# Kernel tuning notes

Measured on AMD Instinct MI355X. Metric: run time of the kernel, lower is better.

The kernel has to match this reference:

```python
import jax, jax.numpy as jnp
import numpy as np

B, N = 4096, 4096
BISECTION_ITERS = 40


def setup_inputs() -> dict:
    key = jax.random.key(0)
    kz, = jax.random.split(key, 1)
    z = jax.random.normal(kz, (B, N), dtype=jnp.float32)
    gamma = jnp.ones((N,), dtype=jnp.float32)   # GammaParam fixed, init=1, clamped at eps (no-op here)
    m = jnp.zeros((N,), dtype=jnp.float32)      # BoundsParam fixed, m_init=0
    M = jnp.ones((N,), dtype=jnp.float32)       # BoundsParam fixed, M_init=1
    xi = jnp.ones((B,), dtype=jnp.float32)      # fixed xi=1 expanded to batch
    return {"z": z, "gamma": gamma, "m": m, "M": M, "xi": xi}


def reference(z, gamma, m, M, xi):
    """Weighted L2 projection of z (B,N) onto {x: sum x = xi, m <= x <= M} via bisection on lambda."""
    Bq, Nq = z.shape
    gB = jnp.broadcast_to(gamma, (Bq, Nq))
    mB = jnp.broadcast_to(m, (Bq, Nq))
    MB = jnp.broadcast_to(M, (Bq, Nq))
    two_gamma = 2.0 * gB

    lam_low = jnp.min(two_gamma * (mB - z), axis=-1)   # (B,)
    lam_high = jnp.max(two_gamma * (MB - z), axis=-1)  # (B,)

    def body(_, carry):
        lo, hi = carry
        mid = 0.5 * (lo + hi)
        x_mid = jnp.clip(z + mid[:, None] / two_gamma, mB, MB)
        g_mid = jnp.sum(x_mid, axis=-1) - xi
        pos = g_mid > 0
        lo_new = jnp.where(pos, lo, mid)
        hi_new = jnp.where(pos, mid, hi)
        return (lo_new, hi_new)

    lam_low, lam_high = jax.lax.fori_loop(0, BISECTION_ITERS, body, (lam_low, lam_high))
    lam = 0.5 * (lam_low + lam_high)
    x = jnp.clip(z + lam[:, None] / two_gamma, mB, MB)
    return x
```

## Files before the change

### kernel.cpp

```cpp
#include <hip/hip_runtime.h>


#define BISECT_STEPS 6
#define TOTAL_STEPS  9

template<int CTRL, int RM>
__device__ __forceinline__ float dpp_add(float v) {
    int t = __builtin_amdgcn_update_dpp(0, __float_as_int(v), CTRL, RM, 0xf, false);
    return v + __int_as_float(t);
}
template<int CTRL, int RM>
__device__ __forceinline__ float dpp_min(float v) {
    int t = __builtin_amdgcn_update_dpp(0x7f800000, __float_as_int(v), CTRL, RM, 0xf, false);
    return fminf(v, __int_as_float(t));
}
template<int CTRL, int RM>
__device__ __forceinline__ float dpp_max(float v) {
    int t = __builtin_amdgcn_update_dpp(0xff800000, __float_as_int(v), CTRL, RM, 0xf, false);
    return fmaxf(v, __int_as_float(t));
}

__device__ __forceinline__ float wave_sum(float v) {
    v = dpp_add<0x111, 0xf>(v);
    v = dpp_add<0x112, 0xf>(v);
    v = dpp_add<0x114, 0xf>(v);
    v = dpp_add<0x118, 0xf>(v);
    v = dpp_add<0x142, 0xa>(v);
    v = dpp_add<0x143, 0xc>(v);
    return __int_as_float(__builtin_amdgcn_readlane(__float_as_int(v), 63));
}
__device__ __forceinline__ float wave_min(float v) {
    v = dpp_min<0x111, 0xf>(v);
    v = dpp_min<0x112, 0xf>(v);
    v = dpp_min<0x114, 0xf>(v);
    v = dpp_min<0x118, 0xf>(v);
    v = dpp_min<0x142, 0xa>(v);
    v = dpp_min<0x143, 0xc>(v);
    return __int_as_float(__builtin_amdgcn_readlane(__float_as_int(v), 63));
}
__device__ __forceinline__ float wave_max(float v) {
    v = dpp_max<0x111, 0xf>(v);
    v = dpp_max<0x112, 0xf>(v);
    v = dpp_max<0x114, 0xf>(v);
    v = dpp_max<0x118, 0xf>(v);
    v = dpp_max<0x142, 0xa>(v);
    v = dpp_max<0x143, 0xc>(v);
    return __int_as_float(__builtin_amdgcn_readlane(__float_as_int(v), 63));
}

__global__ __launch_bounds__(256, 4) void qp_proj_n4096(
    const float* __restrict__ z,
    const float* __restrict__ gamma,
    const float* __restrict__ mlo,
    const float* __restrict__ mhi,
    const float* __restrict__ xi,
    float* __restrict__ out)
{
    constexpr int N = 4096;
    const int row  = blockIdx.x;
    const int tid  = threadIdx.x;
    const int lane = tid & 63;
    const int wid  = tid >> 6;

    const float4* zrow = reinterpret_cast<const float4*>(z + (size_t)row * N);
    const float4* g4   = reinterpret_cast<const float4*>(gamma);
    const float4* m4   = reinterpret_cast<const float4*>(mlo);
    const float4* M4   = reinterpret_cast<const float4*>(mhi);
    float4*       orow = reinterpret_cast<float4*>(out + (size_t)row * N);

    float za[16], ia[16], ma[16], Ma[16];

    float pmin =  INFINITY;
    float pmax = -INFINITY;
    float psm  = 0.0f;
    float psM  = 0.0f;

    #pragma unroll
    for (int k = 0; k < 4; ++k) {
        const int idx = tid + k * 256;
        const float4 zz = zrow[idx];
        const float4 gg = g4[idx];
        const float4 mm = m4[idx];
        const float4 MM = M4[idx];

        const float zs[4] = {zz.x, zz.y, zz.z, zz.w};
        const float gs[4] = {gg.x, gg.y, gg.z, gg.w};
        const float ms[4] = {mm.x, mm.y, mm.z, mm.w};
        const float Ms[4] = {MM.x, MM.y, MM.z, MM.w};

        #pragma unroll
        for (int c = 0; c < 4; ++c) {
            const int j = 4 * k + c;
            const float tg = 2.0f * gs[c];
            za[j] = zs[c];
            ia[j] = 1.0f / tg;
            ma[j] = ms[c];
            Ma[j] = Ms[c];
            pmin = fminf(pmin, tg * (ms[c] - zs[c]));
            pmax = fmaxf(pmax, tg * (Ms[c] - zs[c]));
            psm += ms[c];
            psM += Ms[c];
        }
    }

    __shared__ float wmin[4], wmax[4], wsm[4], wsM[4];
    __shared__ float wsum[2][4];

    pmin = wave_min(pmin);
    pmax = wave_max(pmax);
    psm  = wave_sum(psm);
    psM  = wave_sum(psM);
    if (lane == 0) { wmin[wid] = pmin; wmax[wid] = pmax; wsm[wid] = psm; wsM[wid] = psM; }
    __syncthreads();
    float lo = fminf(fminf(wmin[0], wmin[1]), fminf(wmin[2], wmin[3]));
    float hi = fmaxf(fmaxf(wmax[0], wmax[1]), fmaxf(wmax[2], wmax[3]));

    const float xir = xi[row];
    float glo = (wsm[0] + wsm[1] + wsm[2] + wsm[3]) - xir;
    float ghi = (wsM[0] + wsM[1] + wsM[2] + wsM[3]) - xir;
    int side = 0;

    for (int it = 0; it < TOTAL_STEPS; ++it) {
        const float w = hi - lo;
        float cand;
        if (it < BISECT_STEPS) {
            cand = fmaf(0.5f, w, lo);
        } else {
            const float denom = ghi - glo;
            cand = (lo * ghi - hi * glo) / denom;
            cand = fminf(fmaxf(cand, fmaf(0.0625f, w, lo)),
                         fmaf(-0.0625f, w, hi));
        }

        float t0 = 0.f, t1 = 0.f, t2 = 0.f, t3 = 0.f;
        #pragma unroll
        for (int q = 0; q < 4; ++q) {
            t0 += __builtin_amdgcn_fmed3f(fmaf(cand, ia[4*q+0], za[4*q+0]), ma[4*q+0], Ma[4*q+0]);
            t1 += __builtin_amdgcn_fmed3f(fmaf(cand, ia[4*q+1], za[4*q+1]), ma[4*q+1], Ma[4*q+1]);
            t2 += __builtin_amdgcn_fmed3f(fmaf(cand, ia[4*q+2], za[4*q+2]), ma[4*q+2], Ma[4*q+2]);
            t3 += __builtin_amdgcn_fmed3f(fmaf(cand, ia[4*q+3], za[4*q+3]), ma[4*q+3], Ma[4*q+3]);
        }
        const float sw = wave_sum((t0 + t1) + (t2 + t3));

        const int p = it & 1;
        if (lane == 0) wsum[p][wid] = sw;
        __syncthreads();
        const float s = (wsum[p][0] + wsum[p][1] + wsum[p][2] + wsum[p][3]) - xir;

        if (s > 0.0f) {
            hi = cand;
            if (side == 1) glo *= 0.5f;
            ghi = s;
            side = 1;
        } else {
            lo = cand;
            if (side == -1) ghi *= 0.5f;
            glo = s;
            side = -1;
        }
    }

    const float denom = ghi - glo;
    float lam = (denom > 0.0f) ? (lo * ghi - hi * glo) / denom
                               : fmaf(0.5f, hi - lo, lo);
    lam = fminf(fmaxf(lam, lo), hi);

    #pragma unroll
    for (int k = 0; k < 4; ++k) {
        const int idx = tid + k * 256;
        float4 r;
        float xs[4];
        #pragma unroll
        for (int c = 0; c < 4; ++c) {
            const int j = 4 * k + c;
            const float x = fmaf(lam, ia[j], za[j]);
            xs[c] = __builtin_amdgcn_fmed3f(x, ma[j], Ma[j]);
        }
        r.x = xs[0]; r.y = xs[1]; r.z = xs[2]; r.w = xs[3];
        orow[idx] = r;
    }
}

extern "C" void kernel_launch(void* const* d_in, const int* in_sizes, int n_in,
                              void* d_out, int out_size, void* d_ws, size_t ws_size,
                              hipStream_t stream) {
    const float* z     = (const float*)d_in[0];
    const float* gamma = (const float*)d_in[1];
    const float* m     = (const float*)d_in[2];
    const float* M     = (const float*)d_in[3];
    const float* xi    = (const float*)d_in[4];
    float* out = (float*)d_out;

    const int B = in_sizes[4];
    qp_proj_n4096<<<dim3(B), dim3(256), 0, stream>>>(z, gamma, m, M, xi, out);
}
```

Measured before the change: 34.60 us.

## Reformulate clamp in lambda space and stage per-element bounds in LDS

Rewrites the per-element term clip(z + lam/2g, m, M) as z + med3(lam, lb, hb)/2g, precomputing lb = 2g(m-z) and hb = 2g(M-z). The constant sum of z moves into an adjusted target. The three per-element arrays are kept in shared memory instead of 64 registers per thread, and the occupancy hint in launch bounds is dropped. This cuts register pressure and per-iteration operand count, but adds LDS reads every bisection step, an extra global load of m in the output pass, and a slightly different rounding path for the output.

After: 44.90 us. 29.8% more time.

```diff
diff --git a/kernel.cpp b/kernel.cpp
--- a/kernel.cpp
+++ b/kernel.cpp
@@ -48,7 +48,7 @@
     return __int_as_float(__builtin_amdgcn_readlane(__float_as_int(v), 63));
 }
 
-__global__ __launch_bounds__(256, 4) void qp_proj_n4096(
+__global__ __launch_bounds__(256) void qp_proj_n4096(
     const float* __restrict__ z,
     const float* __restrict__ gamma,
     const float* __restrict__ mlo,
@@ -68,12 +68,17 @@
     const float4* M4   = reinterpret_cast<const float4*>(mhi);
     float4*       orow = reinterpret_cast<float4*>(out + (size_t)row * N);
 
-    float za[16], ia[16], ma[16], Ma[16];
+    __shared__ float4 LB[4][256];
+    __shared__ float4 HB[4][256];
+    __shared__ float4 IA[4][256];
+    __shared__ float  wred[5][4];
+    __shared__ float  wsum[2][4];
 
     float pmin =  INFINITY;
     float pmax = -INFINITY;
     float psm  = 0.0f;
     float psM  = 0.0f;
+    float psz  = 0.0f;
 
     #pragma unroll
     for (int k = 0; k < 4; ++k) {
@@ -88,36 +93,44 @@
         const float ms[4] = {mm.x, mm.y, mm.z, mm.w};
         const float Ms[4] = {MM.x, MM.y, MM.z, MM.w};
 
+        float lb[4], hb[4], ia[4];
         #pragma unroll
         for (int c = 0; c < 4; ++c) {
-            const int j = 4 * k + c;
             const float tg = 2.0f * gs[c];
-            za[j] = zs[c];
-            ia[j] = 1.0f / tg;
-            ma[j] = ms[c];
-            Ma[j] = Ms[c];
-            pmin = fminf(pmin, tg * (ms[c] - zs[c]));
-            pmax = fmaxf(pmax, tg * (Ms[c] - zs[c]));
+            lb[c] = tg * (ms[c] - zs[c]);
+            hb[c] = tg * (Ms[c] - zs[c]);
+            ia[c] = 1.0f / tg;
+            pmin = fminf(pmin, lb[c]);
+            pmax = fmaxf(pmax, hb[c]);
             psm += ms[c];
             psM += Ms[c];
-        }
-    }
-
-    __shared__ float wmin[4], wmax[4], wsm[4], wsM[4];
-    __shared__ float wsum[2][4];
+            psz += zs[c];
+        }
+        LB[k][tid] = make_float4(lb[0], lb[1], lb[2], lb[3]);
+        HB[k][tid] = make_float4(hb[0], hb[1], hb[2], hb[3]);
+        IA[k][tid] = make_float4(ia[0], ia[1], ia[2], ia[3]);
+    }
 
     pmin = wave_min(pmin);
     pmax = wave_max(pmax);
     psm  = wave_sum(psm);
     psM  = wave_sum(psM);
-    if (lane == 0) { wmin[wid] = pmin; wmax[wid] = pmax; wsm[wid] = psm; wsM[wid] = psM; }
+    psz  = wave_sum(psz);
+    if (lane == 0) {
+        wred[0][wid] = pmin; wred[1][wid] = pmax;
+        wred[2][wid] = psm;  wred[3][wid] = psM;  wred[4][wid] = psz;
+    }
     __syncthreads();
-    float lo = fminf(fminf(wmin[0], wmin[1]), fminf(wmin[2], wmin[3]));
-    float hi = fmaxf(fmaxf(wmax[0], wmax[1]), fmaxf(wmax[2], wmax[3]));
-
-    const float xir = xi[row];
-    float glo = (wsm[0] + wsm[1] + wsm[2] + wsm[3]) - xir;
-    float ghi = (wsM[0] + wsM[1] + wsM[2] + wsM[3]) - xir;
+    float lo = fminf(fminf(wred[0][0], wred[0][1]), fminf(wred[0][2], wred[0][3]));
+    float hi = fmaxf(fmaxf(wred[1][0], wred[1][1]), fmaxf(wred[1][2], wred[1][3]));
+    const float smT = (wred[2][0] + wred[2][1]) + (wred[2][2] + wred[2][3]);
+    const float sMT = (wred[3][0] + wred[3][1]) + (wred[3][2] + wred[3][3]);
+    const float szT = (wred[4][0] + wred[4][1]) + (wred[4][2] + wred[4][3]);
+
+    const float xir     = xi[row];
+    const float xir_eff = xir - szT;
+    float glo = smT - xir;
+    float ghi = sMT - xir;
     int side = 0;
 
     for (int it = 0; it < TOTAL_STEPS; ++it) {
@@ -134,18 +147,22 @@
 
         float t0 = 0.f, t1 = 0.f, t2 = 0.f, t3 = 0.f;
         #pragma unroll
-        for (int q = 0; q < 4; ++q) {
-            t0 += __builtin_amdgcn_fmed3f(fmaf(cand, ia[4*q+0], za[4*q+0]), ma[4*q+0], Ma[4*q+0]);
-            t1 += __builtin_amdgcn_fmed3f(fmaf(cand, ia[4*q+1], za[4*q+1]), ma[4*q+1], Ma[4*q+1]);
-            t2 += __builtin_amdgcn_fmed3f(fmaf(cand, ia[4*q+2], za[4*q+2]), ma[4*q+2], Ma[4*q+2]);
-            t3 += __builtin_amdgcn_fmed3f(fmaf(cand, ia[4*q+3], za[4*q+3]), ma[4*q+3], Ma[4*q+3]);
+        for (int k = 0; k < 4; ++k) {
+            const float4 lb = LB[k][tid];
+            const float4 hb = HB[k][tid];
+            const float4 ia = IA[k][tid];
+            t0 = fmaf(ia.x, __builtin_amdgcn_fmed3f(cand, lb.x, hb.x), t0);
+            t1 = fmaf(ia.y, __builtin_amdgcn_fmed3f(cand, lb.y, hb.y), t1);
+            t2 = fmaf(ia.z, __builtin_amdgcn_fmed3f(cand, lb.z, hb.z), t2);
+            t3 = fmaf(ia.w, __builtin_amdgcn_fmed3f(cand, lb.w, hb.w), t3);
         }
         const float sw = wave_sum((t0 + t1) + (t2 + t3));
 
         const int p = it & 1;
         if (lane == 0) wsum[p][wid] = sw;
         __syncthreads();
-        const float s = (wsum[p][0] + wsum[p][1] + wsum[p][2] + wsum[p][3]) - xir;
+        const float s = ((wsum[p][0] + wsum[p][1]) + (wsum[p][2] + wsum[p][3]))
+                        - xir_eff;
 
         if (s > 0.0f) {
             hi = cand;
@@ -168,15 +185,15 @@
     #pragma unroll
     for (int k = 0; k < 4; ++k) {
         const int idx = tid + k * 256;
+        const float4 mm = m4[idx];
+        const float4 lb = LB[k][tid];
+        const float4 hb = HB[k][tid];
+        const float4 ia = IA[k][tid];
         float4 r;
-        float xs[4];
-        #pragma unroll
-        for (int c = 0; c < 4; ++c) {
-            const int j = 4 * k + c;
-            const float x = fmaf(lam, ia[j], za[j]);
-            xs[c] = __builtin_amdgcn_fmed3f(x, ma[j], Ma[j]);
-        }
-        r.x = xs[0]; r.y = xs[1]; r.z = xs[2]; r.w = xs[3];
+        r.x = fmaf(ia.x, __builtin_amdgcn_fmed3f(lam, lb.x, hb.x) - lb.x, mm.x);
+        r.y = fmaf(ia.y, __builtin_amdgcn_fmed3f(lam, lb.y, hb.y) - lb.y, mm.y);
+        r.z = fmaf(ia.z, __builtin_amdgcn_fmed3f(lam, lb.z, hb.z) - lb.z, mm.z);
+        r.w = fmaf(ia.w, __builtin_amdgcn_fmed3f(lam, lb.w, hb.w) - lb.w, mm.w);
         orow[idx] = r;
     }
 }
```

## Specialize for uniform gamma/bounds, process two rows per block with LDS prefetch

Applied to the files above, without the earlier changes.

Adds a pre-pass kernel that checks whether gamma, m and M are uniform across columns and stores the scalar values in the workspace. When they are, the main kernel skips loading the per-column parameter vectors and runs scalar clamps, with the bracket computed from the row min and max of z. It also gives each block two rows: the second row is streamed into LDS with global_load_lds while the first row is reduced, and both rows' reductions share one barrier per step. The step count drops by one, and the fallback path keeps the general per-column behaviour. The risks are an extra memset and launch per call, a coarser solution from one less step, and doubling per-block work, which halves the grid and may hurt occupancy.

Result: slower. 41.04 us (+18.6%).

```diff
diff --git a/kernel.cpp b/kernel.cpp
--- a/kernel.cpp
+++ b/kernel.cpp
@@ -2,182 +2,332 @@
 
 
 #define BISECT_STEPS 6
-#define TOTAL_STEPS  9
+#define TOTAL_STEPS  8
+
+#define GLD_LDS16(gp, lp) __builtin_amdgcn_global_load_lds( \
+    (const __attribute__((address_space(1))) void*)(gp),    \
+    (__attribute__((address_space(3))) void*)(lp), 16, 0, 0)
 
 template<int CTRL, int RM>
-__device__ __forceinline__ float dpp_add(float v) {
+__device__ __forceinline__ float dpp_addf(float v) {
     int t = __builtin_amdgcn_update_dpp(0, __float_as_int(v), CTRL, RM, 0xf, false);
     return v + __int_as_float(t);
 }
 template<int CTRL, int RM>
-__device__ __forceinline__ float dpp_min(float v) {
+__device__ __forceinline__ float dpp_minf(float v) {
     int t = __builtin_amdgcn_update_dpp(0x7f800000, __float_as_int(v), CTRL, RM, 0xf, false);
     return fminf(v, __int_as_float(t));
 }
 template<int CTRL, int RM>
-__device__ __forceinline__ float dpp_max(float v) {
+__device__ __forceinline__ float dpp_maxf(float v) {
     int t = __builtin_amdgcn_update_dpp(0xff800000, __float_as_int(v), CTRL, RM, 0xf, false);
     return fmaxf(v, __int_as_float(t));
 }
-
 __device__ __forceinline__ float wave_sum(float v) {
-    v = dpp_add<0x111, 0xf>(v);
-    v = dpp_add<0x112, 0xf>(v);
-    v = dpp_add<0x114, 0xf>(v);
-    v = dpp_add<0x118, 0xf>(v);
-    v = dpp_add<0x142, 0xa>(v);
-    v = dpp_add<0x143, 0xc>(v);
+    v = dpp_addf<0x111, 0xf>(v);
+    v = dpp_addf<0x112, 0xf>(v);
+    v = dpp_addf<0x114, 0xf>(v);
+    v = dpp_addf<0x118, 0xf>(v);
+    v = dpp_addf<0x142, 0xa>(v);
+    v = dpp_addf<0x143, 0xc>(v);
     return __int_as_float(__builtin_amdgcn_readlane(__float_as_int(v), 63));
 }
 __device__ __forceinline__ float wave_min(float v) {
-    v = dpp_min<0x111, 0xf>(v);
-    v = dpp_min<0x112, 0xf>(v);
-    v = dpp_min<0x114, 0xf>(v);
-    v = dpp_min<0x118, 0xf>(v);
-    v = dpp_min<0x142, 0xa>(v);
-    v = dpp_min<0x143, 0xc>(v);
+    v = dpp_minf<0x111, 0xf>(v);
+    v = dpp_minf<0x112, 0xf>(v);
+    v = dpp_minf<0x114, 0xf>(v);
+    v = dpp_minf<0x118, 0xf>(v);
+    v = dpp_minf<0x142, 0xa>(v);
+    v = dpp_minf<0x143, 0xc>(v);
     return __int_as_float(__builtin_amdgcn_readlane(__float_as_int(v), 63));
 }
 __device__ __forceinline__ float wave_max(float v) {
-    v = dpp_max<0x111, 0xf>(v);
-    v = dpp_max<0x112, 0xf>(v);
-    v = dpp_max<0x114, 0xf>(v);
-    v = dpp_max<0x118, 0xf>(v);
-    v = dpp_max<0x142, 0xa>(v);
-    v = dpp_max<0x143, 0xc>(v);
+    v = dpp_maxf<0x111, 0xf>(v);
+    v = dpp_maxf<0x112, 0xf>(v);
+    v = dpp_maxf<0x114, 0xf>(v);
+    v = dpp_maxf<0x118, 0xf>(v);
+    v = dpp_maxf<0x142, 0xa>(v);
+    v = dpp_maxf<0x143, 0xc>(v);
     return __int_as_float(__builtin_amdgcn_readlane(__float_as_int(v), 63));
 }
 
-__global__ __launch_bounds__(256, 4) void qp_proj_n4096(
+__device__ __forceinline__ float pick_cand(float lo, float hi, float glo,
+                                           float ghi, int it) {
+    const float w = hi - lo;
+    if (it < BISECT_STEPS) return fmaf(0.5f, w, lo);
+    const float denom = ghi - glo;
+    float c = (lo * ghi - hi * glo) / denom;
+    return fminf(fmaxf(c, fmaf(0.0625f, w, lo)), fmaf(-0.0625f, w, hi));
+}
+
+__global__ __launch_bounds__(256) void qp_uniform_check(
+    const float* __restrict__ g, const float* __restrict__ m,
+    const float* __restrict__ M, int n4, void* ws)
+{
+    const int tid = blockIdx.x * 256 + threadIdx.x;
+    const float g0 = g[0], m0 = m[0], M0 = M[0];
+    bool bad = !((g0 > 0.0f) && (M0 >= m0));
+    const float4* g4 = (const float4*)g;
+    const float4* m4 = (const float4*)m;
+    const float4* M4 = (const float4*)M;
+    if (tid < n4) {
+        const float4 a = g4[tid], b = m4[tid], c = M4[tid];
+        bad = bad || (a.x != g0) || (a.y != g0) || (a.z != g0) || (a.w != g0)
+                  || (b.x != m0) || (b.y != m0) || (b.z != m0) || (b.w != m0)
+                  || (c.x != M0) || (c.y != M0) || (c.z != M0) || (c.w != M0);
+    }
+    if (__ballot(bad) != 0ull && (threadIdx.x & 63) == 0)
+        atomicOr((int*)ws, 1);
+    if (tid == 0) {
+        float* wf = (float*)ws;
+        wf[1] = g0; wf[2] = m0; wf[3] = M0;
+    }
+}
+
+__global__ __launch_bounds__(256) void qp_proj2_n4096(
     const float* __restrict__ z,
     const float* __restrict__ gamma,
     const float* __restrict__ mlo,
     const float* __restrict__ mhi,
     const float* __restrict__ xi,
-    float* __restrict__ out)
+    float* __restrict__ out,
+    const void* __restrict__ ws,
+    int Btot)
 {
     constexpr int N = 4096;
-    const int row  = blockIdx.x;
     const int tid  = threadIdx.x;
     const int lane = tid & 63;
     const int wid  = tid >> 6;
-
-    const float4* zrow = reinterpret_cast<const float4*>(z + (size_t)row * N);
-    const float4* g4   = reinterpret_cast<const float4*>(gamma);
-    const float4* m4   = reinterpret_cast<const float4*>(mlo);
-    const float4* M4   = reinterpret_cast<const float4*>(mhi);
-    float4*       orow = reinterpret_cast<float4*>(out + (size_t)row * N);
-
-    float za[16], ia[16], ma[16], Ma[16];
-
-    float pmin =  INFINITY;
-    float pmax = -INFINITY;
-    float psm  = 0.0f;
-    float psM  = 0.0f;
-
+    const int rowA = blockIdx.x * 2;
+    const int rowB = rowA + 1;
+    const bool hasB = (rowB < Btot);
+
+    __shared__ float4 zsB[N / 4];
+    __shared__ float  red[4][4];
+    __shared__ float  wsum[2][2][4];
+
+    const float4* zA4 = reinterpret_cast<const float4*>(z + (size_t)rowA * N);
+    float4* oA4 = reinterpret_cast<float4*>(out + (size_t)rowA * N);
+    float4* oB4 = reinterpret_cast<float4*>(out + (size_t)rowB * N);
+
+    if (hasB) {
+        const char* src = (const char*)(z + (size_t)rowB * N) + tid * 16;
+        char* dst = (char*)zsB + tid * 16;
+        #pragma unroll
+        for (int k = 0; k < 4; ++k)
+            GLD_LDS16(src + k * 4096, dst + k * 4096);
+    }
+
+    float za[16];
+    float amn = INFINITY, amx = -INFINITY;
     #pragma unroll
     for (int k = 0; k < 4; ++k) {
-        const int idx = tid + k * 256;
-        const float4 zz = zrow[idx];
-        const float4 gg = g4[idx];
-        const float4 mm = m4[idx];
-        const float4 MM = M4[idx];
-
-        const float zs[4] = {zz.x, zz.y, zz.z, zz.w};
-        const float gs[4] = {gg.x, gg.y, gg.z, gg.w};
-        const float ms[4] = {mm.x, mm.y, mm.z, mm.w};
-        const float Ms[4] = {MM.x, MM.y, MM.z, MM.w};
-
+        const float4 v = zA4[tid + k * 256];
+        za[4*k+0] = v.x; za[4*k+1] = v.y; za[4*k+2] = v.z; za[4*k+3] = v.w;
+        amn = fminf(amn, fminf(fminf(v.x, v.y), fminf(v.z, v.w)));
+        amx = fmaxf(amx, fmaxf(fmaxf(v.x, v.y), fmaxf(v.z, v.w)));
+    }
+    amn = wave_min(amn);
+    amx = wave_max(amx);
+
+    const int   uniBad = ((const int*)ws)[0];
+    const float g0 = ((const float*)ws)[1];
+    const float m0 = ((const float*)ws)[2];
+    const float M0 = ((const float*)ws)[3];
+    const float xiA = xi[rowA];
+    const float xiB = hasB ? xi[rowB] : 0.0f;
+
+    asm volatile("s_waitcnt vmcnt(0)" ::: "memory");
+    __builtin_amdgcn_sched_barrier(0);
+
+    float bmn = INFINITY, bmx = -INFINITY;
+    if (hasB) {
         #pragma unroll
-        for (int c = 0; c < 4; ++c) {
-            const int j = 4 * k + c;
-            const float tg = 2.0f * gs[c];
-            za[j] = zs[c];
-            ia[j] = 1.0f / tg;
-            ma[j] = ms[c];
-            Ma[j] = Ms[c];
-            pmin = fminf(pmin, tg * (ms[c] - zs[c]));
-            pmax = fmaxf(pmax, tg * (Ms[c] - zs[c]));
-            psm += ms[c];
-            psM += Ms[c];
-        }
-    }
-
-    __shared__ float wmin[4], wmax[4], wsm[4], wsM[4];
-    __shared__ float wsum[2][4];
-
-    pmin = wave_min(pmin);
-    pmax = wave_max(pmax);
-    psm  = wave_sum(psm);
-    psM  = wave_sum(psM);
-    if (lane == 0) { wmin[wid] = pmin; wmax[wid] = pmax; wsm[wid] = psm; wsM[wid] = psM; }
+        for (int k = 0; k < 4; ++k) {
+            const float4 v = zsB[tid + k * 256];
+            bmn = fminf(bmn, fminf(fminf(v.x, v.y), fminf(v.z, v.w)));
+            bmx = fmaxf(bmx, fmaxf(fmaxf(v.x, v.y), fmaxf(v.z, v.w)));
+        }
+    }
+    bmn = wave_min(bmn);
+    bmx = wave_max(bmx);
+    if (lane == 0) { red[0][wid] = amn; red[1][wid] = amx;
+                     red[2][wid] = bmn; red[3][wid] = bmx; }
     __syncthreads();
-    float lo = fminf(fminf(wmin[0], wmin[1]), fminf(wmin[2], wmin[3]));
-    float hi = fmaxf(fmaxf(wmax[0], wmax[1]), fmaxf(wmax[2], wmax[3]));
-
-    const float xir = xi[row];
-    float glo = (wsm[0] + wsm[1] + wsm[2] + wsm[3]) - xir;
-    float ghi = (wsM[0] + wsM[1] + wsM[2] + wsM[3]) - xir;
-    int side = 0;
-
-    for (int it = 0; it < TOTAL_STEPS; ++it) {
-        const float w = hi - lo;
-        float cand;
-        if (it < BISECT_STEPS) {
-            cand = fmaf(0.5f, w, lo);
-        } else {
+    const float zAmin = fminf(fminf(red[0][0], red[0][1]), fminf(red[0][2], red[0][3]));
+    const float zAmax = fmaxf(fmaxf(red[1][0], red[1][1]), fmaxf(red[1][2], red[1][3]));
+    const float zBmin = fminf(fminf(red[2][0], red[2][1]), fminf(red[2][2], red[2][3]));
+    const float zBmax = fmaxf(fmaxf(red[3][0], red[3][1]), fmaxf(red[3][2], red[3][3]));
+
+    if (uniBad == 0) {
+        const float tg = 2.0f * g0;
+        const float ia = 1.0f / tg;
+        const float base_lo = (float)N * m0;
+        const float base_hi = (float)N * M0;
+
+        float loA = tg * (m0 - zAmax), hiA = tg * (M0 - zAmin);
+        float gloA = base_lo - xiA,    ghiA = base_hi - xiA;
+        int sideA = 0;
+        float loB = tg * (m0 - zBmax), hiB = tg * (M0 - zBmin);
+        float gloB = base_lo - xiB,    ghiB = base_hi - xiB;
+        int sideB = 0;
+
+        for (int it = 0; it < TOTAL_STEPS; ++it) {
+            const float cA = pick_cand(loA, hiA, gloA, ghiA, it);
+            const float cB = pick_cand(loB, hiB, gloB, ghiB, it);
+
+            float a0 = 0.f, a1 = 0.f, a2 = 0.f, a3 = 0.f;
+            #pragma unroll
+            for (int q = 0; q < 4; ++q) {
+                a0 += __builtin_amdgcn_fmed3f(fmaf(cA, ia, za[4*q+0]), m0, M0);
+                a1 += __builtin_amdgcn_fmed3f(fmaf(cA, ia, za[4*q+1]), m0, M0);
+                a2 += __builtin_amdgcn_fmed3f(fmaf(cA, ia, za[4*q+2]), m0, M0);
+                a3 += __builtin_amdgcn_fmed3f(fmaf(cA, ia, za[4*q+3]), m0, M0);
+            }
+            float b0 = 0.f, b1 = 0.f, b2 = 0.f, b3 = 0.f;
+            #pragma unroll
+            for (int k = 0; k < 4; ++k) {
+                const float4 v = zsB[tid + k * 256];
+                b0 += __builtin_amdgcn_fmed3f(fmaf(cB, ia, v.x), m0, M0);
+                b1 += __builtin_amdgcn_fmed3f(fmaf(cB, ia, v.y), m0, M0);
+                b2 += __builtin_amdgcn_fmed3f(fmaf(cB, ia, v.z), m0, M0);
+                b3 += __builtin_amdgcn_fmed3f(fmaf(cB, ia, v.w), m0, M0);
+            }
+            const float sA = wave_sum((a0 + a1) + (a2 + a3));
+            const float sB = wave_sum((b0 + b1) + (b2 + b3));
+
+            const int p = it & 1;
+            if (lane == 0) { wsum[p][0][wid] = sA; wsum[p][1][wid] = sB; }
+            __syncthreads();
+            const float gA = ((wsum[p][0][0] + wsum[p][0][1]) + (wsum[p][0][2] + wsum[p][0][3])) - xiA;
+            const float gB = ((wsum[p][1][0] + wsum[p][1][1]) + (wsum[p][1][2] + wsum[p][1][3])) - xiB;
+
+            if (gA > 0.0f) { hiA = cA; if (sideA == 1) gloA *= 0.5f; ghiA = gA; sideA = 1; }
+            else           { loA = cA; if (sideA == -1) ghiA *= 0.5f; gloA = gA; sideA = -1; }
+            if (gB > 0.0f) { hiB = cB; if (sideB == 1) gloB *= 0.5f; ghiB = gB; sideB = 1; }
+            else           { loB = cB; if (sideB == -1) ghiB *= 0.5f; gloB = gB; sideB = -1; }
+        }
+
+        const float dA = ghiA - gloA;
+        float lamA = (dA > 0.0f) ? (loA * ghiA - hiA * gloA) / dA
+                                 : fmaf(0.5f, hiA - loA, loA);
+        lamA = fminf(fmaxf(lamA, loA), hiA);
+        const float dB = ghiB - gloB;
+        float lamB = (dB > 0.0f) ? (loB * ghiB - hiB * gloB) / dB
+                                 : fmaf(0.5f, hiB - loB, loB);
+        lamB = fminf(fmaxf(lamB, loB), hiB);
+
+        #pragma unroll
+        for (int k = 0; k < 4; ++k) {
+            float4 r;
+            r.x = __builtin_amdgcn_fmed3f(fmaf(lamA, ia, za[4*k+0]), m0, M0);
+            r.y = __builtin_amdgcn_fmed3f(fmaf(lamA, ia, za[4*k+1]), m0, M0);
+            r.z = __builtin_amdgcn_fmed3f(fmaf(lamA, ia, za[4*k+2]), m0, M0);
+            r.w = __builtin_amdgcn_fmed3f(fmaf(lamA, ia, za[4*k+3]), m0, M0);
+            oA4[tid + k * 256] = r;
+        }
+        if (hasB) {
+            #pragma unroll
+            for (int k = 0; k < 4; ++k) {
+                const float4 v = zsB[tid + k * 256];
+                float4 r;
+                r.x = __builtin_amdgcn_fmed3f(fmaf(lamB, ia, v.x), m0, M0);
+                r.y = __builtin_amdgcn_fmed3f(fmaf(lamB, ia, v.y), m0, M0);
+                r.z = __builtin_amdgcn_fmed3f(fmaf(lamB, ia, v.z), m0, M0);
+                r.w = __builtin_amdgcn_fmed3f(fmaf(lamB, ia, v.w), m0, M0);
+                oB4[tid + k * 256] = r;
+            }
+        }
+    } else {
+        const float4* g4 = reinterpret_cast<const float4*>(gamma);
+        const float4* m4 = reinterpret_cast<const float4*>(mlo);
+        const float4* M4 = reinterpret_cast<const float4*>(mhi);
+
+        for (int rr = 0; rr < 2; ++rr) {
+            const int row = rowA + rr;
+            if (row >= Btot) break;
+            const float4* zr = reinterpret_cast<const float4*>(z + (size_t)row * N);
+            float4* orow = reinterpret_cast<float4*>(out + (size_t)row * N);
+            const float xir = xi[row];
+
+            float zb[16], ib[16], ma[16], Ma[16];
+            float pmin = INFINITY, pmax = -INFINITY, psm = 0.0f, psM = 0.0f;
+            #pragma unroll
+            for (int k = 0; k < 4; ++k) {
+                const int idx = tid + k * 256;
+                const float4 zz = zr[idx];
+                const float4 gg = g4[idx];
+                const float4 mm = m4[idx];
+                const float4 MM = M4[idx];
+                const float zc[4] = {zz.x, zz.y, zz.z, zz.w};
+                const float gc[4] = {gg.x, gg.y, gg.z, gg.w};
+                const float mc[4] = {mm.x, mm.y, mm.z, mm.w};
+                const float Mc[4] = {MM.x, MM.y, MM.z, MM.w};
+                #pragma unroll
+                for (int c = 0; c < 4; ++c) {
+                    const int j = 4 * k + c;
+                    const float tg2 = 2.0f * gc[c];
+                    zb[j] = zc[c];
+                    ib[j] = 1.0f / tg2;
+                    ma[j] = mc[c];
+                    Ma[j] = Mc[c];
+                    pmin = fminf(pmin, tg2 * (mc[c] - zc[c]));
+                    pmax = fmaxf(pmax, tg2 * (Mc[c] - zc[c]));
+                    psm += mc[c];
+                    psM += Mc[c];
+                }
+            }
+            pmin = wave_min(pmin);
+            pmax = wave_max(pmax);
+            psm  = wave_sum(psm);
+            psM  = wave_sum(psM);
+            if (lane == 0) { red[0][wid] = pmin; red[1][wid] = pmax;
+                             red[2][wid] = psm;  red[3][wid] = psM; }
+            __syncthreads();
+            float lo = fminf(fminf(red[0][0], red[0][1]), fminf(red[0][2], red[0][3]));
+            float hi = fmaxf(fmaxf(red[1][0], red[1][1]), fmaxf(red[1][2], red[1][3]));
+            float glo = ((red[2][0] + red[2][1]) + (red[2][2] + red[2][3])) - xir;
+            float ghi = ((red[3][0] + red[3][1]) + (red[3][2] + red[3][3])) - xir;
+            int side = 0;
+
+            for (int it = 0; it < TOTAL_STEPS + 1; ++it) {
+                const float cand = pick_cand(lo, hi, glo, ghi, it);
+                float t0 = 0.f, t1 = 0.f, t2 = 0.f, t3 = 0.f;
+                #pragma unroll
+                for (int q = 0; q < 4; ++q) {
+                    t0 += __builtin_amdgcn_fmed3f(fmaf(cand, ib[4*q+0], zb[4*q+0]), ma[4*q+0], Ma[4*q+0]);
+                    t1 += __builtin_amdgcn_fmed3f(fmaf(cand, ib[4*q+1], zb[4*q+1]), ma[4*q+1], Ma[4*q+1]);
+                    t2 += __builtin_amdgcn_fmed3f(fmaf(cand, ib[4*q+2], zb[4*q+2]), ma[4*q+2], Ma[4*q+2]);
+                    t3 += __builtin_amdgcn_fmed3f(fmaf(cand, ib[4*q+3], zb[4*q+3]), ma[4*q+3], Ma[4*q+3]);
+                }
+                const float sw = wave_sum((t0 + t1) + (t2 + t3));
+                const int p = it & 1;
+                if (lane == 0) wsum[p][0][wid] = sw;
+                __syncthreads();
+                const float s = ((wsum[p][0][0] + wsum[p][0][1]) + (wsum[p][0][2] + wsum[p][0][3])) - xir;
+                if (s > 0.0f) { hi = cand; if (side == 1) glo *= 0.5f; ghi = s; side = 1; }
+                else          { lo = cand; if (side == -1) ghi *= 0.5f; glo = s; side = -1; }
+            }
+
             const float denom = ghi - glo;
-            cand = (lo * ghi - hi * glo) / denom;
-            cand = fminf(fmaxf(cand, fmaf(0.0625f, w, lo)),
-                         fmaf(-0.0625f, w, hi));
-        }
-
-        float t0 = 0.f, t1 = 0.f, t2 = 0.f, t3 = 0.f;
-        #pragma unroll
-        for (int q = 0; q < 4; ++q) {
-            t0 += __builtin_amdgcn_fmed3f(fmaf(cand, ia[4*q+0], za[4*q+0]), ma[4*q+0], Ma[4*q+0]);
-            t1 += __builtin_amdgcn_fmed3f(fmaf(cand, ia[4*q+1], za[4*q+1]), ma[4*q+1], Ma[4*q+1]);
-            t2 += __builtin_amdgcn_fmed3f(fmaf(cand, ia[4*q+2], za[4*q+2]), ma[4*q+2], Ma[4*q+2]);
-            t3 += __builtin_amdgcn_fmed3f(fmaf(cand, ia[4*q+3], za[4*q+3]), ma[4*q+3], Ma[4*q+3]);
-        }
-        const float sw = wave_sum((t0 + t1) + (t2 + t3));
-
-        const int p = it & 1;
-        if (lane == 0) wsum[p][wid] = sw;
-        __syncthreads();
-        const float s = (wsum[p][0] + wsum[p][1] + wsum[p][2] + wsum[p][3]) - xir;
-
-        if (s > 0.0f) {
-            hi = cand;
-            if (side == 1) glo *= 0.5f;
-            ghi = s;
-            side = 1;
-        } else {
-            lo = cand;
-            if (side == -1) ghi *= 0.5f;
-            glo = s;
-            side = -1;
-        }
-    }
-
-    const float denom = ghi - glo;
-    float lam = (denom > 0.0f) ? (lo * ghi - hi * glo) / denom
-                               : fmaf(0.5f, hi - lo, lo);
-    lam = fminf(fmaxf(lam, lo), hi);
-
-    #pragma unroll
-    for (int k = 0; k < 4; ++k) {
-        const int idx = tid + k * 256;
-        float4 r;
-        float xs[4];
-        #pragma unroll
-        for (int c = 0; c < 4; ++c) {
-            const int j = 4 * k + c;
-            const float x = fmaf(lam, ia[j], za[j]);
-            xs[c] = __builtin_amdgcn_fmed3f(x, ma[j], Ma[j]);
-        }
-        r.x = xs[0]; r.y = xs[1]; r.z = xs[2]; r.w = xs[3];
-        orow[idx] = r;
+            float lam = (denom > 0.0f) ? (lo * ghi - hi * glo) / denom
+                                       : fmaf(0.5f, hi - lo, lo);
+            lam = fminf(fmaxf(lam, lo), hi);
+
+            #pragma unroll
+            for (int k = 0; k < 4; ++k) {
+                float4 r;
+                float xs[4];
+                #pragma unroll
+                for (int c = 0; c < 4; ++c) {
+                    const int j = 4 * k + c;
+                    xs[c] = __builtin_amdgcn_fmed3f(fmaf(lam, ib[j], zb[j]), ma[j], Ma[j]);
+                }
+                r.x = xs[0]; r.y = xs[1]; r.z = xs[2]; r.w = xs[3];
+                orow[tid + k * 256] = r;
+            }
+            __syncthreads();
+        }
     }
 }
 
@@ -192,5 +342,12 @@
     float* out = (float*)d_out;
 
     const int B = in_sizes[4];
-    qp_proj_n4096<<<dim3(B), dim3(256), 0, stream>>>(z, gamma, m, M, xi, out);
-}
+    const int N = in_sizes[1];
+    const int n4 = N / 4;
+
+    hipMemsetAsync(d_ws, 0, 4, stream);
+    qp_uniform_check<<<dim3((n4 + 255) / 256), dim3(256), 0, stream>>>(gamma, m, M, n4, d_ws);
+
+    const int nblocks = (B + 1) / 2;
+    qp_proj2_n4096<<<dim3(nblocks), dim3(256), 0, stream>>>(z, gamma, m, M, xi, out, d_ws, B);
+}
```
